# Kernel tuning notes

Hardware: AMD Instinct MI355X
Metric: run time of the kernel (lower is better)

The kernel has to match this reference:

```python
import jax, jax.numpy as jnp
import numpy as np

N, HIDDEN, D = 4096, 512, 64  # num_stocks, hidden_dim, graph_dim//num_heads
NEG_SLOPE = 0.2


def setup_inputs() -> dict:
    key = jax.random.key(0)
    k1, k2, k3 = jax.random.split(key, 3)
    x = jax.random.normal(k1, (N, HIDDEN), dtype=jnp.float32)
    # fc_transform.weight: Linear(hidden, D, bias=False); stored transposed for x @ W
    W = jax.random.normal(k2, (HIDDEN, D), dtype=jnp.float32) * 0.05
    # fc_attention.weight: Linear(2*D, 1, bias=False) -> vector of length 2*D
    a = jax.random.normal(k3, (2 * D,), dtype=jnp.float32) * 0.05
    return {"x": x, "W": W, "a": a}


def reference(x, W, a):
    # x: (N, hidden) -> transformed features xt: (N, D)
    xt = x @ W
    # The original materializes an (N, N, 2D) tensor of concat([x_i, x_j]) and
    # applies fc_attention. Since fc_attention is linear,
    # a^T [x_i || x_j] = a1 . x_i + a2 . x_j, so we compute scores by broadcast
    # without the N^2 * 2D intermediate.
    a1, a2 = a[:D], a[D:]
    s1 = xt @ a1  # (N,) contribution from row index i
    s2 = xt @ a2  # (N,) contribution from col index j
    e = jax.nn.leaky_relu(s1[:, None] + s2[None, :], NEG_SLOPE)  # (N, N)
    attn = jax.nn.softmax(e, axis=-1)  # softmax over neighbors j
    out = attn @ xt  # einsum 'nm,md->nd'
    return out
```

## Files before the change

### kernel.cpp

```cpp
#include <hip/hip_runtime.h>

#define NN 4096
#define HID 512
#define DD 64
#define SLOPE 0.2f
#define CH 256
#define CL 16

__global__ __launch_bounds__(256) void k1_xt(
    const float* __restrict__ x, const float* __restrict__ W,
    const float* __restrict__ a,
    float* __restrict__ xt, float* __restrict__ s1, float* __restrict__ s2) {
  __shared__ float Wl[HID * DD];
  int tid = threadIdx.x;
  const float4* W4 = (const float4*)W;
  float4* Wl4 = (float4*)Wl;
#pragma unroll
  for (int u = 0; u < (HID * DD / 4) / 256; ++u)
    Wl4[u * 256 + tid] = W4[u * 256 + tid];
  __syncthreads();
  int w = tid >> 6, l = tid & 63;
  int i0 = blockIdx.x * 16 + w * 4;
  const float4* xr0 = (const float4*)(x + (size_t)(i0 + 0) * HID);
  const float4* xr1 = (const float4*)(x + (size_t)(i0 + 1) * HID);
  const float4* xr2 = (const float4*)(x + (size_t)(i0 + 2) * HID);
  const float4* xr3 = (const float4*)(x + (size_t)(i0 + 3) * HID);
  float acc0 = 0.f, acc1 = 0.f, acc2 = 0.f, acc3 = 0.f;
#pragma unroll 2
  for (int k4 = 0; k4 < HID / 4; ++k4) {
    float4 xv0 = xr0[k4], xv1 = xr1[k4], xv2 = xr2[k4], xv3 = xr3[k4];
    int k = k4 * 4;
    float w0 = Wl[(k + 0) * DD + l];
    float w1 = Wl[(k + 1) * DD + l];
    float w2 = Wl[(k + 2) * DD + l];
    float w3 = Wl[(k + 3) * DD + l];
    acc0 = fmaf(xv0.x, w0, acc0); acc0 = fmaf(xv0.y, w1, acc0);
    acc0 = fmaf(xv0.z, w2, acc0); acc0 = fmaf(xv0.w, w3, acc0);
    acc1 = fmaf(xv1.x, w0, acc1); acc1 = fmaf(xv1.y, w1, acc1);
    acc1 = fmaf(xv1.z, w2, acc1); acc1 = fmaf(xv1.w, w3, acc1);
    acc2 = fmaf(xv2.x, w0, acc2); acc2 = fmaf(xv2.y, w1, acc2);
    acc2 = fmaf(xv2.z, w2, acc2); acc2 = fmaf(xv2.w, w3, acc2);
    acc3 = fmaf(xv3.x, w0, acc3); acc3 = fmaf(xv3.y, w1, acc3);
    acc3 = fmaf(xv3.z, w2, acc3); acc3 = fmaf(xv3.w, w3, acc3);
  }
  xt[(i0 + 0) * DD + l] = acc0;
  xt[(i0 + 1) * DD + l] = acc1;
  xt[(i0 + 2) * DD + l] = acc2;
  xt[(i0 + 3) * DD + l] = acc3;
  float a1 = a[l], a2 = a[DD + l];
  float p10 = acc0 * a1, p20 = acc0 * a2;
  float p11 = acc1 * a1, p21 = acc1 * a2;
  float p12 = acc2 * a1, p22 = acc2 * a2;
  float p13 = acc3 * a1, p23 = acc3 * a2;
#pragma unroll
  for (int off = 32; off >= 1; off >>= 1) {
    p10 += __shfl_xor(p10, off, 64); p20 += __shfl_xor(p20, off, 64);
    p11 += __shfl_xor(p11, off, 64); p21 += __shfl_xor(p21, off, 64);
    p12 += __shfl_xor(p12, off, 64); p22 += __shfl_xor(p22, off, 64);
    p13 += __shfl_xor(p13, off, 64); p23 += __shfl_xor(p23, off, 64);
  }
  if (l == 0) {
    s1[i0 + 0] = p10; s2[i0 + 0] = p20;
    s1[i0 + 1] = p11; s2[i0 + 1] = p21;
    s1[i0 + 2] = p12; s2[i0 + 2] = p22;
    s1[i0 + 3] = p13; s2[i0 + 3] = p23;
  }
}

__global__ __launch_bounds__(256) void k2_rank(
    const float* __restrict__ s2, float* __restrict__ s2s, int* __restrict__ perm) {
  __shared__ float keys[NN];
  __shared__ int pc[16][17];
  int tid = threadIdx.x, b = blockIdx.x;
  const float4* s4 = (const float4*)s2;
  float4* kk = (float4*)keys;
#pragma unroll
  for (int u = 0; u < NN / 4 / 256; ++u)
    kk[u * 256 + tid] = s4[u * 256 + tid];
  __syncthreads();
  int el = tid & 15, rep = tid >> 4;
  int e = b * 16 + el;
  float ke = keys[e];
  const float4* k4p = (const float4*)keys;
  int cnt = 0;
#pragma unroll 4
  for (int q4 = rep * 64; q4 < rep * 64 + 64; ++q4) {
    float4 kv = k4p[q4];
    int q = q4 * 4;
    cnt += (kv.x < ke || (kv.x == ke && q + 0 < e)) ? 1 : 0;
    cnt += (kv.y < ke || (kv.y == ke && q + 1 < e)) ? 1 : 0;
    cnt += (kv.z < ke || (kv.z == ke && q + 2 < e)) ? 1 : 0;
    cnt += (kv.w < ke || (kv.w == ke && q + 3 < e)) ? 1 : 0;
  }
  pc[rep][el] = cnt;
  __syncthreads();
  if (tid < 16) {
    int rank = 0;
#pragma unroll
    for (int r = 0; r < 16; ++r) rank += pc[r][tid];
    s2s[rank] = keys[b * 16 + tid];
    perm[rank] = b * 16 + tid;
  }
}

__global__ __launch_bounds__(256) void k3_scan(
    const float* __restrict__ xt, const float* __restrict__ s2s,
    const int* __restrict__ perm,
    float* __restrict__ SP, float* __restrict__ SN,
    float* __restrict__ zP, float* __restrict__ zN) {
  int tid = threadIdx.x, w = tid >> 6, l = tid & 63;
  int cw = blockIdx.x * 4 + w, r0 = cw * CL;
  float evP[CL], evN[CL];
  int pmv[CL];
#pragma unroll
  for (int q = 0; q < CL; ++q) {
    float sv = s2s[r0 + q];
    evP[q] = expf(sv);
    evN[q] = expf(SLOPE * sv);
  }
#pragma unroll
  for (int q = 0; q < CL; ++q) pmv[q] = perm[r0 + q] * DD;
  float aP = 0.f, aN = 0.f, azP = 0.f, azN = 0.f;
#pragma unroll
  for (int q = 0; q < CL; ++q) {
    float xv = xt[pmv[q] + l];
    aP = fmaf(evP[q], xv, aP);
    aN = fmaf(evN[q], xv, aN);
    azP += evP[q]; azN += evN[q];
    SP[(r0 + q) * DD + l] = aP;
    SN[(r0 + q) * DD + l] = aN;
    if (l == 0) { zP[r0 + q] = azP; zN[r0 + q] = azN; }
  }
}

__global__ __launch_bounds__(256) void k4_off(
    const float* __restrict__ SP, const float* __restrict__ SN,
    const float* __restrict__ zP, const float* __restrict__ zN,
    float* __restrict__ offP, float* __restrict__ offN,
    float* __restrict__ offZP, float* __restrict__ offZN) {
  int tid = threadIdx.x, w = tid >> 6, l = tid & 63;
  int gw = blockIdx.x * 4 + w;
  const float* src = nullptr; float* dst = nullptr; int col = 0, stride = 0;
  if (gw < 64)        { src = SP; dst = offP;  col = gw;      stride = DD; }
  else if (gw < 128)  { src = SN; dst = offN;  col = gw - 64; stride = DD; }
  else if (gw == 128) { src = zP; dst = offZP; col = 0;       stride = 1;  }
  else if (gw == 129) { src = zN; dst = offZN; col = 0;       stride = 1;  }
  if (src) {
    int c0 = 4 * l;
    float v0 = src[((c0 + 0) * CL + CL - 1) * stride + col];
    float v1 = src[((c0 + 1) * CL + CL - 1) * stride + col];
    float v2 = src[((c0 + 2) * CL + CL - 1) * stride + col];
    float v3 = src[((c0 + 3) * CL + CL - 1) * stride + col];
    float p1 = v0, p2 = v0 + v1, p3 = v0 + v1 + v2;
    float T = p3 + v3;
    float incl = T;
#pragma unroll
    for (int off = 1; off < 64; off <<= 1) {
      float t2 = __shfl_up(incl, off, 64);
      if (l >= off) incl += t2;
    }
    float excl = incl - T;
    dst[(c0 + 0) * stride + col] = excl;
    dst[(c0 + 1) * stride + col] = excl + p1;
    dst[(c0 + 2) * stride + col] = excl + p2;
    dst[(c0 + 3) * stride + col] = excl + p3;
    if (l == 63) dst[CH * stride + col] = incl;
  }
}

__global__ __launch_bounds__(256) void k5_out(
    const float* __restrict__ s1, const float* __restrict__ s2s,
    const float* __restrict__ SP, const float* __restrict__ SN,
    const float* __restrict__ zP, const float* __restrict__ zN,
    const float* __restrict__ offP, const float* __restrict__ offN,
    const float* __restrict__ offZP, const float* __restrict__ offZN,
    float* __restrict__ out) {
  __shared__ float keys[NN];
  int tid = threadIdx.x, w = tid >> 6, l = tid & 63, b = blockIdx.x;
  const float4* s4 = (const float4*)s2s;
  float4* kk = (float4*)keys;
#pragma unroll
  for (int u = 0; u < NN / 4 / 256; ++u)
    kk[u * 256 + tid] = s4[u * 256 + tid];
  __syncthreads();
  float totP = offP[CH * DD + l];
  float totZ = offZP[CH];
  int q0 = l & 15;
  int i = b * 64 + w * 16 + q0;
  float s1v = s1[i];
  float t = -s1v;
  int lo = 0, hi = NN;
#pragma unroll
  for (int it = 0; it < 12; ++it) {
    int mid = (lo + hi) >> 1;
    if (keys[mid] <= t) lo = mid + 1; else hi = mid;
  }
  int kq = lo;
#pragma unroll
  for (int q = 0; q < 16; ++q) {
    int kk_ = __shfl(kq, q, 64);
    float s1q = __shfl(s1v, q, 64);
    float wPq = expf(s1q);
    float wNq = expf(SLOPE * s1q);
    float FPk = 0.f, FNk = 0.f, ZPk = 0.f, ZNk = 0.f;
    if (kk_ > 0) {
      int r = kk_ - 1, c = r >> 4;
      FPk = offP[c * DD + l] + SP[r * DD + l];
      FNk = offN[c * DD + l] + SN[r * DD + l];
      ZPk = offZP[c] + zP[r];
      ZNk = offZN[c] + zN[r];
    }
    float num = wPq * (totP - FPk) + wNq * FNk;
    float den = wPq * (totZ - ZPk) + wNq * ZNk;
    out[(b * 64 + w * 16 + q) * DD + l] = num / den;
  }
}

extern "C" void kernel_launch(void* const* d_in, const int* in_sizes, int n_in,
                              void* d_out, int out_size, void* d_ws, size_t ws_size,
                              hipStream_t stream) {
  const float* x = (const float*)d_in[0];
  const float* W = (const float*)d_in[1];
  const float* a = (const float*)d_in[2];
  float* out = (float*)d_out;

  float* ws = (float*)d_ws;
  float* xt    = ws;
  float* s1    = xt + NN * DD;
  float* s2    = s1 + NN;
  float* s2s   = s2 + NN;
  int*   perm  = (int*)(s2s + NN);
  float* SP    = (float*)(perm + NN);
  float* SN    = SP + NN * DD;
  float* zP    = SN + NN * DD;
  float* zN    = zP + NN;
  float* offP  = zN + NN;
  float* offN  = offP + (CH + 1) * DD;
  float* offZP = offN + (CH + 1) * DD;
  float* offZN = offZP + (CH + 1);

  k1_xt<<<NN / 16, 256, 0, stream>>>(x, W, a, xt, s1, s2);
  k2_rank<<<NN / 16, 256, 0, stream>>>(s2, s2s, perm);
  k3_scan<<<CH / 4, 256, 0, stream>>>(xt, s2s, perm, SP, SN, zP, zN);
  k4_off<<<33, 256, 0, stream>>>(SP, SN, zP, zN, offP, offN, offZP, offZN);
  k5_out<<<NN / 64, 256, 0, stream>>>(s1, s2s, SP, SN, zP, zN,
                                      offP, offN, offZP, offZN, out);
}
```

Baseline: 51.97 us.

## Shrink scan chunks, halve k1 LDS footprint, spread k5 over more blocks

Scan chunk length drops from 16 to 4 rows, so the chunk count rises from 256 to 1024. k3 gets four times as many waves, k4 does a 16-element serial prefix per lane, and k5 launches four times as many blocks, each handling 16 rows. k1 now stages W through shared memory in two 64KB halves instead of one 128KB copy, which cuts LDS use per block and should allow more resident blocks. k3 also issues its gathered xt loads before the FMA chain. In exchange, k5 blocks reload the 16KB key array four times as often, and k1 adds an extra barrier.

```diff
diff --git a/kernel.cpp b/kernel.cpp
--- a/kernel.cpp
+++ b/kernel.cpp
@@ -4,21 +4,15 @@
 #define HID 512
 #define DD 64
 #define SLOPE 0.2f
-#define CH 256
-#define CL 16
+#define CH 1024
+#define CL 4
 
 __global__ __launch_bounds__(256) void k1_xt(
     const float* __restrict__ x, const float* __restrict__ W,
     const float* __restrict__ a,
     float* __restrict__ xt, float* __restrict__ s1, float* __restrict__ s2) {
-  __shared__ float Wl[HID * DD];
+  __shared__ float Wl[256 * DD];
   int tid = threadIdx.x;
-  const float4* W4 = (const float4*)W;
-  float4* Wl4 = (float4*)Wl;
-#pragma unroll
-  for (int u = 0; u < (HID * DD / 4) / 256; ++u)
-    Wl4[u * 256 + tid] = W4[u * 256 + tid];
-  __syncthreads();
   int w = tid >> 6, l = tid & 63;
   int i0 = blockIdx.x * 16 + w * 4;
   const float4* xr0 = (const float4*)(x + (size_t)(i0 + 0) * HID);
@@ -26,22 +20,33 @@
   const float4* xr2 = (const float4*)(x + (size_t)(i0 + 2) * HID);
   const float4* xr3 = (const float4*)(x + (size_t)(i0 + 3) * HID);
   float acc0 = 0.f, acc1 = 0.f, acc2 = 0.f, acc3 = 0.f;
+#pragma unroll
+  for (int half = 0; half < 2; ++half) {
+    __syncthreads();
+    const float4* W4 = (const float4*)(W + half * 256 * DD);
+    float4* Wl4 = (float4*)Wl;
+#pragma unroll
+    for (int u = 0; u < (256 * DD / 4) / 256; ++u)
+      Wl4[u * 256 + tid] = W4[u * 256 + tid];
+    __syncthreads();
 #pragma unroll 2
-  for (int k4 = 0; k4 < HID / 4; ++k4) {
-    float4 xv0 = xr0[k4], xv1 = xr1[k4], xv2 = xr2[k4], xv3 = xr3[k4];
-    int k = k4 * 4;
-    float w0 = Wl[(k + 0) * DD + l];
-    float w1 = Wl[(k + 1) * DD + l];
-    float w2 = Wl[(k + 2) * DD + l];
-    float w3 = Wl[(k + 3) * DD + l];
-    acc0 = fmaf(xv0.x, w0, acc0); acc0 = fmaf(xv0.y, w1, acc0);
-    acc0 = fmaf(xv0.z, w2, acc0); acc0 = fmaf(xv0.w, w3, acc0);
-    acc1 = fmaf(xv1.x, w0, acc1); acc1 = fmaf(xv1.y, w1, acc1);
-    acc1 = fmaf(xv1.z, w2, acc1); acc1 = fmaf(xv1.w, w3, acc1);
-    acc2 = fmaf(xv2.x, w0, acc2); acc2 = fmaf(xv2.y, w1, acc2);
-    acc2 = fmaf(xv2.z, w2, acc2); acc2 = fmaf(xv2.w, w3, acc2);
-    acc3 = fmaf(xv3.x, w0, acc3); acc3 = fmaf(xv3.y, w1, acc3);
-    acc3 = fmaf(xv3.z, w2, acc3); acc3 = fmaf(xv3.w, w3, acc3);
+    for (int k4 = 0; k4 < 64; ++k4) {
+      int kg = half * 64 + k4;
+      float4 xv0 = xr0[kg], xv1 = xr1[kg], xv2 = xr2[kg], xv3 = xr3[kg];
+      int k = k4 * 4;
+      float w0 = Wl[(k + 0) * DD + l];
+      float w1 = Wl[(k + 1) * DD + l];
+      float w2 = Wl[(k + 2) * DD + l];
+      float w3 = Wl[(k + 3) * DD + l];
+      acc0 = fmaf(xv0.x, w0, acc0); acc0 = fmaf(xv0.y, w1, acc0);
+      acc0 = fmaf(xv0.z, w2, acc0); acc0 = fmaf(xv0.w, w3, acc0);
+      acc1 = fmaf(xv1.x, w0, acc1); acc1 = fmaf(xv1.y, w1, acc1);
+      acc1 = fmaf(xv1.z, w2, acc1); acc1 = fmaf(xv1.w, w3, acc1);
+      acc2 = fmaf(xv2.x, w0, acc2); acc2 = fmaf(xv2.y, w1, acc2);
+      acc2 = fmaf(xv2.z, w2, acc2); acc2 = fmaf(xv2.w, w3, acc2);
+      acc3 = fmaf(xv3.x, w0, acc3); acc3 = fmaf(xv3.y, w1, acc3);
+      acc3 = fmaf(xv3.z, w2, acc3); acc3 = fmaf(xv3.w, w3, acc3);
+    }
   }
   xt[(i0 + 0) * DD + l] = acc0;
   xt[(i0 + 1) * DD + l] = acc1;
@@ -110,7 +115,7 @@
     float* __restrict__ zP, float* __restrict__ zN) {
   int tid = threadIdx.x, w = tid >> 6, l = tid & 63;
   int cw = blockIdx.x * 4 + w, r0 = cw * CL;
-  float evP[CL], evN[CL];
+  float evP[CL], evN[CL], xv[CL];
   int pmv[CL];
 #pragma unroll
   for (int q = 0; q < CL; ++q) {
@@ -120,12 +125,13 @@
   }
 #pragma unroll
   for (int q = 0; q < CL; ++q) pmv[q] = perm[r0 + q] * DD;
+#pragma unroll
+  for (int q = 0; q < CL; ++q) xv[q] = xt[pmv[q] + l];
   float aP = 0.f, aN = 0.f, azP = 0.f, azN = 0.f;
 #pragma unroll
   for (int q = 0; q < CL; ++q) {
-    float xv = xt[pmv[q] + l];
-    aP = fmaf(evP[q], xv, aP);
-    aN = fmaf(evN[q], xv, aN);
+    aP = fmaf(evP[q], xv[q], aP);
+    aN = fmaf(evN[q], xv[q], aN);
     azP += evP[q]; azN += evN[q];
     SP[(r0 + q) * DD + l] = aP;
     SN[(r0 + q) * DD + l] = aN;
@@ -146,13 +152,15 @@
   else if (gw == 128) { src = zP; dst = offZP; col = 0;       stride = 1;  }
   else if (gw == 129) { src = zN; dst = offZN; col = 0;       stride = 1;  }
   if (src) {
-    int c0 = 4 * l;
-    float v0 = src[((c0 + 0) * CL + CL - 1) * stride + col];
-    float v1 = src[((c0 + 1) * CL + CL - 1) * stride + col];
-    float v2 = src[((c0 + 2) * CL + CL - 1) * stride + col];
-    float v3 = src[((c0 + 3) * CL + CL - 1) * stride + col];
-    float p1 = v0, p2 = v0 + v1, p3 = v0 + v1 + v2;
-    float T = p3 + v3;
+    int c0 = 16 * l;
+    float v[16], p[16];
+#pragma unroll
+    for (int j = 0; j < 16; ++j)
+      v[j] = src[((c0 + j) * CL + CL - 1) * stride + col];
+    float run = 0.f;
+#pragma unroll
+    for (int j = 0; j < 16; ++j) { p[j] = run; run += v[j]; }
+    float T = run;
     float incl = T;
 #pragma unroll
     for (int off = 1; off < 64; off <<= 1) {
@@ -160,10 +168,9 @@
       if (l >= off) incl += t2;
     }
     float excl = incl - T;
-    dst[(c0 + 0) * stride + col] = excl;
-    dst[(c0 + 1) * stride + col] = excl + p1;
-    dst[(c0 + 2) * stride + col] = excl + p2;
-    dst[(c0 + 3) * stride + col] = excl + p3;
+#pragma unroll
+    for (int j = 0; j < 16; ++j)
+      dst[(c0 + j) * stride + col] = excl + p[j];
     if (l == 63) dst[CH * stride + col] = incl;
   }
 }
@@ -185,8 +192,8 @@
   __syncthreads();
   float totP = offP[CH * DD + l];
   float totZ = offZP[CH];
-  int q0 = l & 15;
-  int i = b * 64 + w * 16 + q0;
+  int q0 = l & 3;
+  int i = b * 16 + w * 4 + q0;
   float s1v = s1[i];
   float t = -s1v;
   int lo = 0, hi = NN;
@@ -197,14 +204,14 @@
   }
   int kq = lo;
 #pragma unroll
-  for (int q = 0; q < 16; ++q) {
+  for (int q = 0; q < 4; ++q) {
     int kk_ = __shfl(kq, q, 64);
     float s1q = __shfl(s1v, q, 64);
     float wPq = expf(s1q);
     float wNq = expf(SLOPE * s1q);
     float FPk = 0.f, FNk = 0.f, ZPk = 0.f, ZNk = 0.f;
     if (kk_ > 0) {
-      int r = kk_ - 1, c = r >> 4;
+      int r = kk_ - 1, c = r >> 2;
       FPk = offP[c * DD + l] + SP[r * DD + l];
       FNk = offN[c * DD + l] + SN[r * DD + l];
       ZPk = offZP[c] + zP[r];
@@ -212,7 +219,7 @@
     }
     float num = wPq * (totP - FPk) + wNq * FNk;
     float den = wPq * (totZ - ZPk) + wNq * ZNk;
-    out[(b * 64 + w * 16 + q) * DD + l] = num / den;
+    out[(b * 16 + w * 4 + q) * DD + l] = num / den;
   }
 }
 
@@ -243,6 +250,6 @@
   k2_rank<<<NN / 16, 256, 0, stream>>>(s2, s2s, perm);
   k3_scan<<<CH / 4, 256, 0, stream>>>(xt, s2s, perm, SP, SN, zP, zN);
   k4_off<<<33, 256, 0, stream>>>(SP, SN, zP, zN, offP, offN, offZP, offZN);
-  k5_out<<<NN / 64, 256, 0, stream>>>(s1, s2s, SP, SN, zP, zN,
+  k5_out<<<NN / 16, 256, 0, stream>>>(s1, s2s, SP, SN, zP, zN,
                                       offP, offN, offZP, offZN, out);
 }
```

Result: faster. 46.74 us (-10.1%).
